# Performance work log

Hardware: AMD Instinct MI355X
Metric: run time of the kernel (lower is better)

The kernel has to match this reference:

```python
import jax, jax.numpy as jnp
import numpy as np

N = 100000
E = 1600000
HID = 128


def gcn_conv(x, W, b, src, dst, n):
    # PyG GCNConv: h = X W; add self-loops; D^{-1/2}(A+I)D^{-1/2} h + b
    h = x @ W                                   # [n, out]
    loop = jnp.arange(n)
    s = jnp.concatenate([src, loop])            # sources incl. self-loops
    d = jnp.concatenate([dst, loop])            # targets incl. self-loops
    deg = jax.ops.segment_sum(jnp.ones(s.shape[0], dtype=h.dtype), d, num_segments=n)
    dinv = jnp.where(deg > 0, jax.lax.rsqrt(deg), 0.0)
    norm = dinv[s] * dinv[d]                    # [E+n]
    out = jax.ops.segment_sum(h[s] * norm[:, None], d, num_segments=n)
    return out + b


def setup_inputs() -> dict:
    key = jax.random.key(0)
    ks = jax.random.split(key, 16)
    coords = jax.random.normal(ks[0], (N, 2), dtype=jnp.float32)
    edge_index = jax.random.randint(ks[1], (2, E), 0, N, dtype=jnp.int64)

    def lin(k, fin, fout):
        k1, k2 = jax.random.split(k)
        s = 1.0 / np.sqrt(fin)
        W = jax.random.uniform(k1, (fin, fout), jnp.float32, -s, s)
        b = jax.random.uniform(k2, (fout,), jnp.float32, -s, s)
        return W, b

    W1, b1 = lin(ks[2], 3, HID)
    W2, b2 = lin(ks[3], HID, HID)
    Ws, bs = lin(ks[4], HID, 1)
    Wmu, bmu = lin(ks[5], HID, 2)
    Wls, bls = lin(ks[6], HID, 2)
    Wv1, bv1 = lin(ks[7], HID, 64)
    Wv2, bv2 = lin(ks[8], 64, 1)
    return {"coords": coords, "edge_index": edge_index,
            "W1": W1, "b1": b1, "W2": W2, "b2": b2,
            "Ws": Ws, "bs": bs, "Wmu": Wmu, "bmu": bmu,
            "Wls": Wls, "bls": bls, "Wv1": Wv1, "bv1": bv1,
            "Wv2": Wv2, "bv2": bv2}


def reference(coords, edge_index, W1, b1, W2, b2, Ws, bs, Wmu, bmu, Wls, bls, Wv1, bv1, Wv2, bv2):
    n = coords.shape[0]
    src, dst = edge_index[0], edge_index[1]
    # degree feature (no self-loops), normalized by max degree
    degree = jax.ops.segment_sum(jnp.ones(src.shape[0], dtype=jnp.float32), src, num_segments=n)
    degree = degree / jnp.maximum(degree.max(), 1.0)
    x = jnp.concatenate([coords, degree[:, None]], axis=1)  # [N, 3]
    x = jax.nn.relu(gcn_conv(x, W1, b1, src, dst, n))       # [N, HID]
    x = jax.nn.relu(gcn_conv(x, W2, b2, src, dst, n))       # [N, HID]
    node_logits = jax.nn.log_softmax((x @ Ws + bs).squeeze(-1), axis=0)  # [N]
    mu = x @ Wmu + bmu                                      # [N, 2]
    log_std = jnp.clip(x @ Wls + bls, -4.0, 2.0)            # [N, 2]
    g = x.mean(axis=0)                                      # [HID]
    value = (jax.nn.relu(g @ Wv1 + bv1) @ Wv2 + bv2).squeeze()
    return node_logits, mu, log_std, value
```

## Files before the change

### kernel.cpp

```cpp
#include <hip/hip_runtime.h>
#include <hip/hip_bf16.h>

#define HID 128
#define NB2MAX 128

typedef __bf16 bf16x8 __attribute__((ext_vector_type(8)));
typedef float f32x4 __attribute__((ext_vector_type(4)));
typedef float f32x2 __attribute__((ext_vector_type(2)));

#if defined(__has_builtin)
#if __has_builtin(__builtin_amdgcn_cvt_pk_f32_fp8) && __has_builtin(__builtin_amdgcn_cvt_pk_fp8_f32)
#define HAVE_FP8_CVT 1
#endif
#endif
#ifndef HAVE_FP8_CVT
#define HAVE_FP8_CVT 0
#include <hip/hip_fp8.h>
#endif

__device__ __forceinline__ float b2f(unsigned int u) { return __uint_as_float(u << 16); }
__device__ __forceinline__ unsigned int f2b(float f) {
  unsigned int b = __float_as_uint(f);
  return (b + 0x7FFFu + ((b >> 16) & 1u)) >> 16;
}
__device__ __forceinline__ unsigned int pack2(float lo, float hi) {
  return f2b(lo) | (f2b(hi) << 16);
}

#if !HAVE_FP8_CVT
__device__ __forceinline__ float fp8dec(unsigned int u) {
  unsigned int e = (u >> 3) & 15, m = u & 7, sgn = (u >> 7) & 1;
  float v;
  if (e) v = __uint_as_float(((e + 120) << 23) | (m << 20));
  else v = (float)m * 0.001953125f;
  return sgn ? -v : v;
}
#endif

__device__ __forceinline__ unsigned int pk4_fp8(float v0, float v1, float v2, float v3) {
#if HAVE_FP8_CVT
  int pk = 0;
  pk = __builtin_amdgcn_cvt_pk_fp8_f32(v0, v1, pk, false);
  pk = __builtin_amdgcn_cvt_pk_fp8_f32(v2, v3, pk, true);
  return (unsigned int)pk;
#else
  __hip_fp8_e4m3 a(v0), b(v1), c(v2), d(v3);
  return (unsigned)a.__x | ((unsigned)b.__x << 8) | ((unsigned)c.__x << 16) |
         ((unsigned)d.__x << 24);
#endif
}

__device__ __forceinline__ void acc4_fp8(unsigned int u, float* a) {
#if HAVE_FP8_CVT
  f32x2 lo = __builtin_amdgcn_cvt_pk_f32_fp8((int)u, false);
  f32x2 hi = __builtin_amdgcn_cvt_pk_f32_fp8((int)u, true);
  a[0] += lo.x; a[1] += lo.y; a[2] += hi.x; a[3] += hi.y;
#else
  a[0] += fp8dec(u & 255); a[1] += fp8dec((u >> 8) & 255);
  a[2] += fp8dec((u >> 16) & 255); a[3] += fp8dec((u >> 24) & 255);
#endif
}

__global__ void k_scatter2(const int* __restrict__ src, const int* __restrict__ dst, int E,
                           int NB2, int CAP, int* __restrict__ curd, int* __restrict__ curs,
                           int* __restrict__ pairsp, unsigned short* __restrict__ srcb) {
  __shared__ int hd[NB2MAX], hs[NB2MAX], bd[NB2MAX], bs[NB2MAX];
  for (int i = threadIdx.x; i < NB2; i += 256) { hd[i] = 0; hs[i] = 0; }
  __syncthreads();
  int per = (E + gridDim.x - 1) / gridDim.x;
  int begin = blockIdx.x * per;
  int end = min(E, begin + per);
  for (int e = begin + threadIdx.x; e < end; e += 256) {
    atomicAdd(&hd[dst[e] >> 10], 1);
    atomicAdd(&hs[src[e] >> 10], 1);
  }
  __syncthreads();
  for (int i = threadIdx.x; i < NB2; i += 256) {
    bd[i] = hd[i] ? atomicAdd(&curd[i], hd[i]) : 0;
    bs[i] = hs[i] ? atomicAdd(&curs[i], hs[i]) : 0;
    hd[i] = 0; hs[i] = 0;
  }
  __syncthreads();
  for (int e = begin + threadIdx.x; e < end; e += 256) {
    int d = dst[e], s = src[e];
    int bD = d >> 10, bS = s >> 10;
    int offD = bd[bD] + atomicAdd(&hd[bD], 1);
    if (offD < CAP) pairsp[(size_t)bD * CAP + offD] = (s << 10) | (d & 1023);
    int offS = bs[bS] + atomicAdd(&hs[bS], 1);
    if (offS < CAP) srcb[(size_t)bS * CAP + offS] = (unsigned short)(s & 1023);
  }
}

__global__ __launch_bounds__(1024) void k_degcsr(
    const unsigned short* __restrict__ srcb, const int* __restrict__ curs,
    const int* __restrict__ pairsp, const int* __restrict__ curd, int NB2, int CAP, int N,
    int* __restrict__ degsrc, int* __restrict__ bmax, int2* __restrict__ rowptr2,
    float* __restrict__ dinv, int* __restrict__ colarr) {
  __shared__ int cnt[1024], scn[1024], cur[1024];
  int tid = threadIdx.x;
  if ((int)blockIdx.x < NB2) {
    int b = blockIdx.x;
    int g = (b << 10) + tid;
    int lo = b * CAP;
    cnt[tid] = 0; __syncthreads();
    int szS = min(curs[b], CAP);
    const unsigned short* sb = srcb + (size_t)lo;
    for (int k = tid; k < szS; k += 1024) atomicAdd(&cnt[sb[k]], 1);
    __syncthreads();
    int c = cnt[tid];
    if (g < N) degsrc[g] = c;
    scn[tid] = (g < N) ? c : 0; __syncthreads();
    for (int s = 512; s > 0; s >>= 1) {
      if (tid < s) scn[tid] = max(scn[tid], scn[tid + s]);
      __syncthreads();
    }
    if (tid == 0) bmax[b] = scn[0];
    return;
  }
  int b = blockIdx.x - NB2;
  int g = (b << 10) + tid;
  int lo = b * CAP;
  cnt[tid] = 0; __syncthreads();
  int szD = min(curd[b], CAP);
  const int* pb = pairsp + (size_t)lo;
  for (int k = tid; k < szD; k += 1024) atomicAdd(&cnt[pb[k] & 1023], 1);
  __syncthreads();
  int c = cnt[tid];
  scn[tid] = c; __syncthreads();
  for (int st = 1; st < 1024; st <<= 1) {
    int t = (tid >= st) ? scn[tid - st] : 0;
    __syncthreads();
    scn[tid] += t;
    __syncthreads();
  }
  int excl = scn[tid] - c;
  if (g < N) {
    rowptr2[g] = make_int2(lo + excl, lo + excl + c);
    dinv[g] = rsqrtf((float)(c + 1));
  }
  cur[tid] = lo + excl;
  __syncthreads();
  for (int k = tid; k < szD; k += 1024) {
    int p = pb[k];
    int pos = atomicAdd(&cur[p & 1023], 1);
    colarr[pos] = ((unsigned)p) >> 10;
  }
}

__global__ void k_prepW(const float* __restrict__ W2, unsigned short* __restrict__ W2T) {
  int idx = blockIdx.x * 256 + threadIdx.x;
  if (idx >= 128 * 128) return;
  int j = idx >> 7, k = idx & 127;
  W2T[j * 128 + k] = (unsigned short)f2b(W2[k * 128 + j]);
}

__global__ void k_node(const float* __restrict__ coords, const int* __restrict__ degsrc,
                       const float* __restrict__ dinv, const int* __restrict__ bmax, int NB2,
                       int N, float4* __restrict__ x0s) {
  __shared__ int sm[128];
  int tid = threadIdx.x;
  if (tid < 128) sm[tid] = (tid < NB2) ? bmax[tid] : 0;
  __syncthreads();
  if (tid < 64) { sm[tid] = max(sm[tid], sm[tid + 64]); }
  __syncthreads();
  if (tid < 32) { sm[tid] = max(sm[tid], sm[tid + 32]); }
  __syncthreads();
  if (tid < 16) { sm[tid] = max(sm[tid], sm[tid + 16]); }
  __syncthreads();
  if (tid < 8) { sm[tid] = max(sm[tid], sm[tid + 8]); }
  __syncthreads();
  if (tid < 4) { sm[tid] = max(sm[tid], sm[tid + 4]); }
  __syncthreads();
  if (tid < 2) { sm[tid] = max(sm[tid], sm[tid + 2]); }
  __syncthreads();
  if (tid == 0) sm[0] = max(sm[0], sm[1]);
  __syncthreads();
  float inv = 1.0f / (float)max(sm[0], 1);
  int n = blockIdx.x * 256 + tid;
  if (n >= N) return;
  float di = dinv[n];
  float4 v;
  v.x = coords[n * 2 + 0] * di;
  v.y = coords[n * 2 + 1] * di;
  v.z = (float)degsrc[n] * inv * di;
  v.w = 0.f;
  x0s[n] = v;
}

__global__ void k_agg3lin(const float4* __restrict__ x0s, const float* __restrict__ dinv,
                          const int2* __restrict__ rowptr2, const int* __restrict__ col,
                          const float* __restrict__ W1, const float* __restrict__ b1, int N,
                          unsigned int* __restrict__ x1f8) {
  __shared__ float w0s[128], w1s[128], w2s[128], bsm[128];
  for (int t = threadIdx.x; t < 128; t += 256) {
    w0s[t] = W1[t];
    w1s[t] = W1[128 + t];
    w2s[t] = W1[256 + t];
    bsm[t] = b1[t];
  }
  __syncthreads();
  int n = blockIdx.x * 256 + threadIdx.x;
  if (n >= N) return;
  float4 a = x0s[n];
  int2 rp = rowptr2[n];
  int k = rp.x, en = rp.y;
  for (; k + 3 < en; k += 4) {
    int s0 = col[k], s1 = col[k + 1], s2 = col[k + 2], s3 = col[k + 3];
    float4 w0 = x0s[s0];
    float4 w1 = x0s[s1];
    float4 w2 = x0s[s2];
    float4 w3 = x0s[s3];
    a.x += (w0.x + w1.x) + (w2.x + w3.x);
    a.y += (w0.y + w1.y) + (w2.y + w3.y);
    a.z += (w0.z + w1.z) + (w2.z + w3.z);
  }
  for (; k < en; k++) {
    float4 w = x0s[col[k]];
    a.x += w.x; a.y += w.y; a.z += w.z;
  }
  float di = dinv[n];
  float ax = a.x * di, ay = a.y * di, az = a.z * di;
  unsigned int* orow = x1f8 + (size_t)n * 32;
#pragma unroll 8
  for (int f0 = 0; f0 < 128; f0 += 4) {
    float v0 = fmaxf(bsm[f0] + ax * w0s[f0] + ay * w1s[f0] + az * w2s[f0], 0.f) * di;
    float v1 = fmaxf(bsm[f0 + 1] + ax * w0s[f0 + 1] + ay * w1s[f0 + 1] + az * w2s[f0 + 1], 0.f) * di;
    float v2 = fmaxf(bsm[f0 + 2] + ax * w0s[f0 + 2] + ay * w1s[f0 + 2] + az * w2s[f0 + 2], 0.f) * di;
    float v3 = fmaxf(bsm[f0 + 3] + ax * w0s[f0 + 3] + ay * w1s[f0 + 3] + az * w2s[f0 + 3], 0.f) * di;
    orow[f0 >> 2] = pk4_fp8(v0, v1, v2, v3);
  }
}

__global__ void k_agg128(const unsigned int* __restrict__ x1f8, const float* __restrict__ dinv,
                         const int2* __restrict__ rowptr2, const int* __restrict__ col,
                         int N, unsigned short* __restrict__ xa) {
  int g = (int)((blockIdx.x * 256 + threadIdx.x) >> 3);
  int lane = threadIdx.x & 7;
  if (g >= N) return;
  const uint4* base = (const uint4*)x1f8 + lane;
  float acc[16];
#pragma unroll
  for (int i = 0; i < 16; i++) acc[i] = 0.f;
  uint4 self = base[(size_t)g * 8];
  acc4_fp8(self.x, acc); acc4_fp8(self.y, acc + 4);
  acc4_fp8(self.z, acc + 8); acc4_fp8(self.w, acc + 12);
  int2 rp = rowptr2[g];
  int k = rp.x, en = rp.y;
  for (; k + 3 < en; k += 4) {
    int s0 = col[k], s1 = col[k + 1], s2 = col[k + 2], s3 = col[k + 3];
    uint4 w0 = base[(size_t)s0 * 8];
    uint4 w1 = base[(size_t)s1 * 8];
    uint4 w2 = base[(size_t)s2 * 8];
    uint4 w3 = base[(size_t)s3 * 8];
    acc4_fp8(w0.x, acc); acc4_fp8(w0.y, acc + 4); acc4_fp8(w0.z, acc + 8); acc4_fp8(w0.w, acc + 12);
    acc4_fp8(w1.x, acc); acc4_fp8(w1.y, acc + 4); acc4_fp8(w1.z, acc + 8); acc4_fp8(w1.w, acc + 12);
    acc4_fp8(w2.x, acc); acc4_fp8(w2.y, acc + 4); acc4_fp8(w2.z, acc + 8); acc4_fp8(w2.w, acc + 12);
    acc4_fp8(w3.x, acc); acc4_fp8(w3.y, acc + 4); acc4_fp8(w3.z, acc + 8); acc4_fp8(w3.w, acc + 12);
  }
  for (; k < en; k++) {
    uint4 w = base[(size_t)col[k] * 8];
    acc4_fp8(w.x, acc); acc4_fp8(w.y, acc + 4); acc4_fp8(w.z, acc + 8); acc4_fp8(w.w, acc + 12);
  }
  float di = dinv[g];
  uint4 o1, o2;
  o1.x = pack2(acc[0] * di, acc[1] * di);
  o1.y = pack2(acc[2] * di, acc[3] * di);
  o1.z = pack2(acc[4] * di, acc[5] * di);
  o1.w = pack2(acc[6] * di, acc[7] * di);
  o2.x = pack2(acc[8] * di, acc[9] * di);
  o2.y = pack2(acc[10] * di, acc[11] * di);
  o2.z = pack2(acc[12] * di, acc[13] * di);
  o2.w = pack2(acc[14] * di, acc[15] * di);
  uint4* op = (uint4*)xa + (size_t)g * 16 + lane * 2;
  op[0] = o1;
  op[1] = o2;
}

__global__ __launch_bounds__(256) void k_gemm2(const unsigned short* __restrict__ xab,
                                               const unsigned short* __restrict__ W2T,
                                               const float* __restrict__ b2,
                                               const float* __restrict__ Ws,
                                               const float* __restrict__ bs,
                                               const float* __restrict__ Wmu,
                                               const float* __restrict__ bmu,
                                               const float* __restrict__ Wls,
                                               const float* __restrict__ bls,
                                               int N, float* __restrict__ s_arr,
                                               float* __restrict__ out,
                                               float* __restrict__ partials) {
  __shared__ float w[640];
  __shared__ float cs[4][128];
  for (int t = threadIdx.x; t < 128; t += 256) {
    w[t] = Ws[t];
    w[128 + t] = Wmu[t * 2 + 0];
    w[256 + t] = Wmu[t * 2 + 1];
    w[384 + t] = Wls[t * 2 + 0];
    w[512 + t] = Wls[t * 2 + 1];
  }
  __syncthreads();
  int wv = threadIdx.x >> 6;
  int lane = threadIdx.x & 63;
  int l15 = lane & 15, lhi = lane >> 4;
  int rowbase = blockIdx.x * 64 + wv * 16;
  int arow = rowbase + l15;
  int arowc = min(arow, N - 1);
  const unsigned short* ap = xab + (size_t)arowc * HID + lhi * 8;
  bf16x8 a[4];
#pragma unroll
  for (int kk = 0; kk < 4; kk++) a[kk] = *(const bf16x8*)(ap + kk * 32);
  float cpart[8];
  float p0[4] = {0, 0, 0, 0}, p1[4] = {0, 0, 0, 0}, p2[4] = {0, 0, 0, 0};
  float p3[4] = {0, 0, 0, 0}, p4[4] = {0, 0, 0, 0};
#pragma unroll
  for (int ct = 0; ct < 8; ct++) {
    f32x4 acc = {0.f, 0.f, 0.f, 0.f};
    const unsigned short* bp = W2T + (size_t)(ct * 16 + l15) * HID + lhi * 8;
#pragma unroll
    for (int kk = 0; kk < 4; kk++) {
      bf16x8 bfr = *(const bf16x8*)(bp + kk * 32);
      acc = __builtin_amdgcn_mfma_f32_16x16x32_bf16(a[kk], bfr, acc, 0, 0, 0);
    }
    int cidx = ct * 16 + l15;
    float bias = b2[cidx];
    float ws_ = w[cidx];
    float wm0 = w[128 + cidx], wm1 = w[256 + cidx];
    float wl0 = w[384 + cidx], wl1 = w[512 + cidx];
    float cl = 0.f;
#pragma unroll
    for (int r = 0; r < 4; r++) {
      int node = rowbase + lhi * 4 + r;
      float o = fmaxf(acc[r] + bias, 0.f);
      if (node < N) cl += o;
      p0[r] += o * ws_;
      p1[r] += o * wm0;
      p2[r] += o * wm1;
      p3[r] += o * wl0;
      p4[r] += o * wl1;
    }
    cl += __shfl_xor(cl, 16);
    cl += __shfl_xor(cl, 32);
    cpart[ct] = cl;
  }
#pragma unroll
  for (int r = 0; r < 4; r++) {
#pragma unroll
    for (int m = 1; m < 16; m <<= 1) {
      p0[r] += __shfl_xor(p0[r], m);
      p1[r] += __shfl_xor(p1[r], m);
      p2[r] += __shfl_xor(p2[r], m);
      p3[r] += __shfl_xor(p3[r], m);
      p4[r] += __shfl_xor(p4[r], m);
    }
  }
  if (l15 == 0) {
#pragma unroll
    for (int r = 0; r < 4; r++) {
      int node = rowbase + lhi * 4 + r;
      if (node < N) {
        s_arr[node] = p0[r] + bs[0];
        out[(size_t)N + node * 2 + 0] = p1[r] + bmu[0];
        out[(size_t)N + node * 2 + 1] = p2[r] + bmu[1];
        out[(size_t)3 * N + node * 2 + 0] = fminf(fmaxf(p3[r] + bls[0], -4.f), 2.f);
        out[(size_t)3 * N + node * 2 + 1] = fminf(fmaxf(p4[r] + bls[1], -4.f), 2.f);
      }
    }
  }
  if (lane < 16) {
#pragma unroll
    for (int ct = 0; ct < 8; ct++) cs[wv][ct * 16 + lane] = cpart[ct];
  }
  __syncthreads();
  if (threadIdx.x < 128) {
    int f = threadIdx.x;
    partials[(size_t)blockIdx.x * 128 + f] = cs[0][f] + cs[1][f] + cs[2][f] + cs[3][f];
  }
}

__global__ void k_lse_colsum(const float* __restrict__ s, int N, float* __restrict__ pm,
                             float* __restrict__ pt, const float* __restrict__ partials,
                             int nblkG, float* __restrict__ colsum) {
  if (blockIdx.x >= 256) {
    int bb = blockIdx.x - 256;
    int f = threadIdx.x;
    if (f < 128) {
      float t = 0.f;
      for (int b = bb; b < nblkG; b += 64) t += partials[(size_t)b * 128 + f];
      atomicAdd(&colsum[f], t);
    }
    return;
  }
  __shared__ float smM[256], smT[256];
  float m = -1e30f, t = 0.f;
  for (int i = blockIdx.x * 256 + threadIdx.x; i < N; i += 256 * 256) {
    float v = s[i];
    if (v > m) { t = t * __expf(m - v) + 1.f; m = v; }
    else t += __expf(v - m);
  }
  smM[threadIdx.x] = m; smT[threadIdx.x] = t; __syncthreads();
  for (int st = 128; st > 0; st >>= 1) {
    if (threadIdx.x < st) {
      float m2 = smM[threadIdx.x + st], t2 = smT[threadIdx.x + st];
      float m1 = smM[threadIdx.x], t1 = smT[threadIdx.x];
      float M = fmaxf(m1, m2);
      smM[threadIdx.x] = M;
      smT[threadIdx.x] = t1 * __expf(m1 - M) + t2 * __expf(m2 - M);
    }
    __syncthreads();
  }
  if (threadIdx.x == 0) { pm[blockIdx.x] = smM[0]; pt[blockIdx.x] = smT[0]; }
}

__global__ void k_logits_value(const float* __restrict__ sarr, const float* __restrict__ pm,
                               const float* __restrict__ pt, int N, float* __restrict__ out,
                               const float* __restrict__ colsum, const float* __restrict__ Wv1,
                               const float* __restrict__ bv1, const float* __restrict__ Wv2,
                               const float* __restrict__ bv2, int nblkN) {
  if ((int)blockIdx.x == nblkN) {
    __shared__ float hid[64];
    float invN = 1.0f / (float)N;
    int j = threadIdx.x;
    if (j < 64) {
      float a = bv1[j];
      for (int f = 0; f < 128; f++) a += (colsum[f] * invN) * Wv1[f * 64 + j];
      hid[j] = fmaxf(a, 0.f) * Wv2[j];
    }
    __syncthreads();
    if (threadIdx.x == 0) {
      float v = bv2[0];
      for (int jj = 0; jj < 64; jj++) v += hid[jj];
      out[(size_t)5 * N] = v;
    }
    return;
  }
  __shared__ float smM[256], smT[256];
  smM[threadIdx.x] = pm[threadIdx.x];
  smT[threadIdx.x] = pt[threadIdx.x];
  __syncthreads();
  for (int st = 128; st > 0; st >>= 1) {
    if (threadIdx.x < st) {
      float m2 = smM[threadIdx.x + st], t2 = smT[threadIdx.x + st];
      float m1 = smM[threadIdx.x], t1 = smT[threadIdx.x];
      float M = fmaxf(m1, m2);
      smM[threadIdx.x] = M;
      smT[threadIdx.x] = t1 * __expf(m1 - M) + t2 * __expf(m2 - M);
    }
    __syncthreads();
  }
  float lse = smM[0] + logf(smT[0]);
  int n = blockIdx.x * 256 + threadIdx.x;
  if (n < N) out[n] = sarr[n] - lse;
}

extern "C" void kernel_launch(void* const* d_in, const int* in_sizes, int n_in,
                              void* d_out, int out_size, void* d_ws, size_t ws_size,
                              hipStream_t stream) {
  const float* coords = (const float*)d_in[0];
  const int* ei = (const int*)d_in[1];
  const float* W1 = (const float*)d_in[2];
  const float* b1 = (const float*)d_in[3];
  const float* W2 = (const float*)d_in[4];
  const float* b2 = (const float*)d_in[5];
  const float* Wsw = (const float*)d_in[6];
  const float* bsw = (const float*)d_in[7];
  const float* Wmu = (const float*)d_in[8];
  const float* bmu = (const float*)d_in[9];
  const float* Wls = (const float*)d_in[10];
  const float* bls = (const float*)d_in[11];
  const float* Wv1 = (const float*)d_in[12];
  const float* bv1 = (const float*)d_in[13];
  const float* Wv2 = (const float*)d_in[14];
  const float* bv2 = (const float*)d_in[15];
  int N = in_sizes[0] / 2;
  int E = in_sizes[1] / 2;
  const int* src = ei;
  const int* dst = ei + E;
  float* outf = (float*)d_out;
  int NB2 = (N + 1023) >> 10;
  int CAP = ((E / NB2) * 5 / 4 + 1024 + 255) & ~255;
  int nblkG = (N + 63) / 64;
  int nblkN = (N + 255) / 256;

  char* base = (char*)d_ws;
  size_t off = 0;
  auto alloc = [&](size_t bytes) -> void* {
    void* r = base + off;
    off += (bytes + 255) & ~(size_t)255;
    return r;
  };
  size_t zero_start = off;
  int* curd = (int*)alloc((size_t)NB2 * 4);
  int* curs = (int*)alloc((size_t)NB2 * 4);
  float* colsum = (float*)alloc(128 * 4);
  size_t zero_bytes = off - zero_start;
  int* bmax = (int*)alloc((size_t)NB2 * 4);
  int2* rowptr2 = (int2*)alloc((size_t)N * 8);
  int* pairsp = (int*)alloc((size_t)NB2 * CAP * 4);
  unsigned short* srcb = (unsigned short*)alloc((size_t)NB2 * CAP * 2);
  int* colarr = (int*)alloc((size_t)NB2 * CAP * 4);
  int* degsrc = (int*)alloc((size_t)N * 4);
  float* dinv = (float*)alloc((size_t)N * 4);
  float4* x0s = (float4*)alloc((size_t)N * 16);
  float* sarr = (float*)alloc((size_t)N * 4);
  float* pm = (float*)alloc(256 * 4);
  float* pt = (float*)alloc(256 * 4);
  unsigned short* W2T = (unsigned short*)alloc(128 * 128 * 2);
  float* partials = (float*)alloc((size_t)nblkG * 128 * 4);
  unsigned int* x1f8 = (unsigned int*)alloc((size_t)N * 128);
  unsigned short* xab = (unsigned short*)alloc((size_t)N * HID * 2);
  if (off > ws_size) return;

  hipMemsetAsync(base + zero_start, 0, zero_bytes, stream);
  k_scatter2<<<512, 256, 0, stream>>>(src, dst, E, NB2, CAP, curd, curs, pairsp, srcb);
  k_degcsr<<<2 * NB2, 1024, 0, stream>>>(srcb, curs, pairsp, curd, NB2, CAP, N, degsrc, bmax,
                                         rowptr2, dinv, colarr);
  k_prepW<<<64, 256, 0, stream>>>(W2, W2T);
  k_node<<<nblkN, 256, 0, stream>>>(coords, degsrc, dinv, bmax, NB2, N, x0s);
  k_agg3lin<<<nblkN, 256, 0, stream>>>(x0s, dinv, rowptr2, colarr, W1, b1, N, x1f8);
  k_agg128<<<(N * 8 + 255) / 256, 256, 0, stream>>>(x1f8, dinv, rowptr2, colarr, N, xab);
  k_gemm2<<<nblkG, 256, 0, stream>>>(xab, W2T, b2, Wsw, bsw, Wmu, bmu, Wls, bls, N, sarr, outf,
                                     partials);
  k_lse_colsum<<<320, 256, 0, stream>>>(sarr, N, pm, pt, partials, nblkG, colsum);
  k_logits_value<<<nblkN + 1, 256, 0, stream>>>(sarr, pm, pt, N, outf, colsum, Wv1, bv1, Wv2,
                                                bv2, nblkN);
}
```

Measured before the change: 165.1 us.

## Fuse layer-2 neighbor aggregation with MFMA GEMM and heads via shared memory

```diff
diff --git a/kernel.cpp b/kernel.cpp
--- a/kernel.cpp
+++ b/kernel.cpp
@@ -231,65 +231,18 @@
   }
 }
 
-__global__ void k_agg128(const unsigned int* __restrict__ x1f8, const float* __restrict__ dinv,
-                         const int2* __restrict__ rowptr2, const int* __restrict__ col,
-                         int N, unsigned short* __restrict__ xa) {
-  int g = (int)((blockIdx.x * 256 + threadIdx.x) >> 3);
-  int lane = threadIdx.x & 7;
-  if (g >= N) return;
-  const uint4* base = (const uint4*)x1f8 + lane;
-  float acc[16];
-#pragma unroll
-  for (int i = 0; i < 16; i++) acc[i] = 0.f;
-  uint4 self = base[(size_t)g * 8];
-  acc4_fp8(self.x, acc); acc4_fp8(self.y, acc + 4);
-  acc4_fp8(self.z, acc + 8); acc4_fp8(self.w, acc + 12);
-  int2 rp = rowptr2[g];
-  int k = rp.x, en = rp.y;
-  for (; k + 3 < en; k += 4) {
-    int s0 = col[k], s1 = col[k + 1], s2 = col[k + 2], s3 = col[k + 3];
-    uint4 w0 = base[(size_t)s0 * 8];
-    uint4 w1 = base[(size_t)s1 * 8];
-    uint4 w2 = base[(size_t)s2 * 8];
-    uint4 w3 = base[(size_t)s3 * 8];
-    acc4_fp8(w0.x, acc); acc4_fp8(w0.y, acc + 4); acc4_fp8(w0.z, acc + 8); acc4_fp8(w0.w, acc + 12);
-    acc4_fp8(w1.x, acc); acc4_fp8(w1.y, acc + 4); acc4_fp8(w1.z, acc + 8); acc4_fp8(w1.w, acc + 12);
-    acc4_fp8(w2.x, acc); acc4_fp8(w2.y, acc + 4); acc4_fp8(w2.z, acc + 8); acc4_fp8(w2.w, acc + 12);
-    acc4_fp8(w3.x, acc); acc4_fp8(w3.y, acc + 4); acc4_fp8(w3.z, acc + 8); acc4_fp8(w3.w, acc + 12);
-  }
-  for (; k < en; k++) {
-    uint4 w = base[(size_t)col[k] * 8];
-    acc4_fp8(w.x, acc); acc4_fp8(w.y, acc + 4); acc4_fp8(w.z, acc + 8); acc4_fp8(w.w, acc + 12);
-  }
-  float di = dinv[g];
-  uint4 o1, o2;
-  o1.x = pack2(acc[0] * di, acc[1] * di);
-  o1.y = pack2(acc[2] * di, acc[3] * di);
-  o1.z = pack2(acc[4] * di, acc[5] * di);
-  o1.w = pack2(acc[6] * di, acc[7] * di);
-  o2.x = pack2(acc[8] * di, acc[9] * di);
-  o2.y = pack2(acc[10] * di, acc[11] * di);
-  o2.z = pack2(acc[12] * di, acc[13] * di);
-  o2.w = pack2(acc[14] * di, acc[15] * di);
-  uint4* op = (uint4*)xa + (size_t)g * 16 + lane * 2;
-  op[0] = o1;
-  op[1] = o2;
-}
-
-__global__ __launch_bounds__(256) void k_gemm2(const unsigned short* __restrict__ xab,
-                                               const unsigned short* __restrict__ W2T,
-                                               const float* __restrict__ b2,
-                                               const float* __restrict__ Ws,
-                                               const float* __restrict__ bs,
-                                               const float* __restrict__ Wmu,
-                                               const float* __restrict__ bmu,
-                                               const float* __restrict__ Wls,
-                                               const float* __restrict__ bls,
-                                               int N, float* __restrict__ s_arr,
-                                               float* __restrict__ out,
-                                               float* __restrict__ partials) {
+__global__ __launch_bounds__(256) void k_aggemm(
+    const unsigned int* __restrict__ x1f8, const float* __restrict__ dinv,
+    const int2* __restrict__ rowptr2, const int* __restrict__ col,
+    const unsigned short* __restrict__ W2T, const float* __restrict__ b2,
+    const float* __restrict__ Ws, const float* __restrict__ bs,
+    const float* __restrict__ Wmu, const float* __restrict__ bmu,
+    const float* __restrict__ Wls, const float* __restrict__ bls,
+    int N, float* __restrict__ s_arr, float* __restrict__ out,
+    float* __restrict__ partials) {
   __shared__ float w[640];
-  __shared__ float cs[4][128];
+  __shared__ unsigned short xs[32 * 136];
+  __shared__ float cs[2][128];
   for (int t = threadIdx.x; t < 128; t += 256) {
     w[t] = Ws[t];
     w[128 + t] = Wmu[t * 2 + 0];
@@ -297,82 +250,126 @@
     w[384 + t] = Wls[t * 2 + 0];
     w[512 + t] = Wls[t * 2 + 1];
   }
+  int nloc = threadIdx.x >> 3;
+  int lane8 = threadIdx.x & 7;
+  int g = blockIdx.x * 32 + nloc;
+  uint4 o1 = make_uint4(0, 0, 0, 0), o2 = make_uint4(0, 0, 0, 0);
+  if (g < N) {
+    const uint4* base = (const uint4*)x1f8 + lane8;
+    float acc[16];
+#pragma unroll
+    for (int i = 0; i < 16; i++) acc[i] = 0.f;
+    uint4 self = base[(size_t)g * 8];
+    acc4_fp8(self.x, acc); acc4_fp8(self.y, acc + 4);
+    acc4_fp8(self.z, acc + 8); acc4_fp8(self.w, acc + 12);
+    int2 rp = rowptr2[g];
+    int k = rp.x, en = rp.y;
+    for (; k + 3 < en; k += 4) {
+      int s0 = col[k], s1 = col[k + 1], s2 = col[k + 2], s3 = col[k + 3];
+      uint4 w0 = base[(size_t)s0 * 8];
+      uint4 w1 = base[(size_t)s1 * 8];
+      uint4 w2 = base[(size_t)s2 * 8];
+      uint4 w3 = base[(size_t)s3 * 8];
+      acc4_fp8(w0.x, acc); acc4_fp8(w0.y, acc + 4); acc4_fp8(w0.z, acc + 8); acc4_fp8(w0.w, acc + 12);
+      acc4_fp8(w1.x, acc); acc4_fp8(w1.y, acc + 4); acc4_fp8(w1.z, acc + 8); acc4_fp8(w1.w, acc + 12);
+      acc4_fp8(w2.x, acc); acc4_fp8(w2.y, acc + 4); acc4_fp8(w2.z, acc + 8); acc4_fp8(w2.w, acc + 12);
+      acc4_fp8(w3.x, acc); acc4_fp8(w3.y, acc + 4); acc4_fp8(w3.z, acc + 8); acc4_fp8(w3.w, acc + 12);
+    }
+    for (; k < en; k++) {
+      uint4 wq = base[(size_t)col[k] * 8];
+      acc4_fp8(wq.x, acc); acc4_fp8(wq.y, acc + 4); acc4_fp8(wq.z, acc + 8); acc4_fp8(wq.w, acc + 12);
+    }
+    float di = dinv[g];
+    o1.x = pack2(acc[0] * di, acc[1] * di);
+    o1.y = pack2(acc[2] * di, acc[3] * di);
+    o1.z = pack2(acc[4] * di, acc[5] * di);
+    o1.w = pack2(acc[6] * di, acc[7] * di);
+    o2.x = pack2(acc[8] * di, acc[9] * di);
+    o2.y = pack2(acc[10] * di, acc[11] * di);
+    o2.z = pack2(acc[12] * di, acc[13] * di);
+    o2.w = pack2(acc[14] * di, acc[15] * di);
+  }
+  {
+    uint4* xrow = (uint4*)(xs + nloc * 136 + lane8 * 16);
+    xrow[0] = o1;
+    xrow[1] = o2;
+  }
   __syncthreads();
   int wv = threadIdx.x >> 6;
-  int lane = threadIdx.x & 63;
-  int l15 = lane & 15, lhi = lane >> 4;
-  int rowbase = blockIdx.x * 64 + wv * 16;
-  int arow = rowbase + l15;
-  int arowc = min(arow, N - 1);
-  const unsigned short* ap = xab + (size_t)arowc * HID + lhi * 8;
-  bf16x8 a[4];
-#pragma unroll
-  for (int kk = 0; kk < 4; kk++) a[kk] = *(const bf16x8*)(ap + kk * 32);
-  float cpart[8];
-  float p0[4] = {0, 0, 0, 0}, p1[4] = {0, 0, 0, 0}, p2[4] = {0, 0, 0, 0};
-  float p3[4] = {0, 0, 0, 0}, p4[4] = {0, 0, 0, 0};
-#pragma unroll
-  for (int ct = 0; ct < 8; ct++) {
-    f32x4 acc = {0.f, 0.f, 0.f, 0.f};
-    const unsigned short* bp = W2T + (size_t)(ct * 16 + l15) * HID + lhi * 8;
-#pragma unroll
-    for (int kk = 0; kk < 4; kk++) {
-      bf16x8 bfr = *(const bf16x8*)(bp + kk * 32);
-      acc = __builtin_amdgcn_mfma_f32_16x16x32_bf16(a[kk], bfr, acc, 0, 0, 0);
-    }
-    int cidx = ct * 16 + l15;
-    float bias = b2[cidx];
-    float ws_ = w[cidx];
-    float wm0 = w[128 + cidx], wm1 = w[256 + cidx];
-    float wl0 = w[384 + cidx], wl1 = w[512 + cidx];
-    float cl = 0.f;
+  if (wv < 2) {
+    int lane = threadIdx.x & 63;
+    int l15 = lane & 15, lhi = lane >> 4;
+    int rowbase = blockIdx.x * 32 + wv * 16;
+    const unsigned short* ap = xs + (wv * 16 + l15) * 136 + lhi * 8;
+    bf16x8 a[4];
+#pragma unroll
+    for (int kk = 0; kk < 4; kk++) a[kk] = *(const bf16x8*)(ap + kk * 32);
+    float cpart[8];
+    float p0[4] = {0, 0, 0, 0}, p1[4] = {0, 0, 0, 0}, p2[4] = {0, 0, 0, 0};
+    float p3[4] = {0, 0, 0, 0}, p4[4] = {0, 0, 0, 0};
+#pragma unroll
+    for (int ct = 0; ct < 8; ct++) {
+      f32x4 acc = {0.f, 0.f, 0.f, 0.f};
+      const unsigned short* bp = W2T + (size_t)(ct * 16 + l15) * HID + lhi * 8;
+#pragma unroll
+      for (int kk = 0; kk < 4; kk++) {
+        bf16x8 bfr = *(const bf16x8*)(bp + kk * 32);
+        acc = __builtin_amdgcn_mfma_f32_16x16x32_bf16(a[kk], bfr, acc, 0, 0, 0);
+      }
+      int cidx = ct * 16 + l15;
+      float bias = b2[cidx];
+      float ws_ = w[cidx];
+      float wm0 = w[128 + cidx], wm1 = w[256 + cidx];
+      float wl0 = w[384 + cidx], wl1 = w[512 + cidx];
+      float cl = 0.f;
+#pragma unroll
+      for (int r = 0; r < 4; r++) {
+        int node = rowbase + lhi * 4 + r;
+        float o = fmaxf(acc[r] + bias, 0.f);
+        if (node < N) cl += o;
+        p0[r] += o * ws_;
+        p1[r] += o * wm0;
+        p2[r] += o * wm1;
+        p3[r] += o * wl0;
+        p4[r] += o * wl1;
+      }
+      cl += __shfl_xor(cl, 16);
+      cl += __shfl_xor(cl, 32);
+      cpart[ct] = cl;
+    }
 #pragma unroll
     for (int r = 0; r < 4; r++) {
-      int node = rowbase + lhi * 4 + r;
-      float o = fmaxf(acc[r] + bias, 0.f);
-      if (node < N) cl += o;
-      p0[r] += o * ws_;
-      p1[r] += o * wm0;
-      p2[r] += o * wm1;
-      p3[r] += o * wl0;
-      p4[r] += o * wl1;
-    }
-    cl += __shfl_xor(cl, 16);
-    cl += __shfl_xor(cl, 32);
-    cpart[ct] = cl;
-  }
-#pragma unroll
-  for (int r = 0; r < 4; r++) {
-#pragma unroll
-    for (int m = 1; m < 16; m <<= 1) {
-      p0[r] += __shfl_xor(p0[r], m);
-      p1[r] += __shfl_xor(p1[r], m);
-      p2[r] += __shfl_xor(p2[r], m);
-      p3[r] += __shfl_xor(p3[r], m);
-      p4[r] += __shfl_xor(p4[r], m);
-    }
-  }
-  if (l15 == 0) {
-#pragma unroll
-    for (int r = 0; r < 4; r++) {
-      int node = rowbase + lhi * 4 + r;
-      if (node < N) {
-        s_arr[node] = p0[r] + bs[0];
-        out[(size_t)N + node * 2 + 0] = p1[r] + bmu[0];
-        out[(size_t)N + node * 2 + 1] = p2[r] + bmu[1];
-        out[(size_t)3 * N + node * 2 + 0] = fminf(fmaxf(p3[r] + bls[0], -4.f), 2.f);
-        out[(size_t)3 * N + node * 2 + 1] = fminf(fmaxf(p4[r] + bls[1], -4.f), 2.f);
+#pragma unroll
+      for (int m = 1; m < 16; m <<= 1) {
+        p0[r] += __shfl_xor(p0[r], m);
+        p1[r] += __shfl_xor(p1[r], m);
+        p2[r] += __shfl_xor(p2[r], m);
+        p3[r] += __shfl_xor(p3[r], m);
+        p4[r] += __shfl_xor(p4[r], m);
       }
     }
-  }
-  if (lane < 16) {
-#pragma unroll
-    for (int ct = 0; ct < 8; ct++) cs[wv][ct * 16 + lane] = cpart[ct];
+    if (l15 == 0) {
+#pragma unroll
+      for (int r = 0; r < 4; r++) {
+        int node = rowbase + lhi * 4 + r;
+        if (node < N) {
+          s_arr[node] = p0[r] + bs[0];
+          out[(size_t)N + node * 2 + 0] = p1[r] + bmu[0];
+          out[(size_t)N + node * 2 + 1] = p2[r] + bmu[1];
+          out[(size_t)3 * N + node * 2 + 0] = fminf(fmaxf(p3[r] + bls[0], -4.f), 2.f);
+          out[(size_t)3 * N + node * 2 + 1] = fminf(fmaxf(p4[r] + bls[1], -4.f), 2.f);
+        }
+      }
+    }
+    if (lane < 16) {
+#pragma unroll
+      for (int ct = 0; ct < 8; ct++) cs[wv][ct * 16 + lane] = cpart[ct];
+    }
   }
   __syncthreads();
   if (threadIdx.x < 128) {
     int f = threadIdx.x;
-    partials[(size_t)blockIdx.x * 128 + f] = cs[0][f] + cs[1][f] + cs[2][f] + cs[3][f];
+    partials[(size_t)blockIdx.x * 128 + f] = cs[0][f] + cs[1][f];
   }
 }
 
@@ -477,7 +474,7 @@
   float* outf = (float*)d_out;
   int NB2 = (N + 1023) >> 10;
   int CAP = ((E / NB2) * 5 / 4 + 1024 + 255) & ~255;
-  int nblkG = (N + 63) / 64;
+  int nblkG = (N + 31) / 32;
   int nblkN = (N + 255) / 256;
 
   char* base = (char*)d_ws;
@@ -506,7 +503,6 @@
   unsigned short* W2T = (unsigned short*)alloc(128 * 128 * 2);
   float* partials = (float*)alloc((size_t)nblkG * 128 * 4);
   unsigned int* x1f8 = (unsigned int*)alloc((size_t)N * 128);
-  unsigned short* xab = (unsigned short*)alloc((size_t)N * HID * 2);
   if (off > ws_size) return;
 
   hipMemsetAsync(base + zero_start, 0, zero_bytes, stream);
@@ -516,9 +512,8 @@
   k_prepW<<<64, 256, 0, stream>>>(W2, W2T);
   k_node<<<nblkN, 256, 0, stream>>>(coords, degsrc, dinv, bmax, NB2, N, x0s);
   k_agg3lin<<<nblkN, 256, 0, stream>>>(x0s, dinv, rowptr2, colarr, W1, b1, N, x1f8);
-  k_agg128<<<(N * 8 + 255) / 256, 256, 0, stream>>>(x1f8, dinv, rowptr2, colarr, N, xab);
-  k_gemm2<<<nblkG, 256, 0, stream>>>(xab, W2T, b2, Wsw, bsw, Wmu, bmu, Wls, bls, N, sarr, outf,
-                                     partials);
+  k_aggemm<<<nblkG, 256, 0, stream>>>(x1f8, dinv, rowptr2, colarr, W2T, b2, Wsw, bsw, Wmu, bmu,
+                                      Wls, bls, N, sarr, outf, partials);
   k_lse_colsum<<<320, 256, 0, stream>>>(sarr, N, pm, pt, partials, nblkG, colsum);
   k_logits_value<<<nblkN + 1, 256, 0, stream>>>(sarr, pm, pt, N, outf, colsum, Wv1, bv1, Wv2,
                                                 bv2, nblkN);
```

Result: slower. 171.4 us (+3.8%).
